# Optimization experiments

Hardware: AMD Instinct MI355X
Metric: run time of the kernel (lower is better)

The kernel has to match this reference:

```python
import math
import jax, jax.numpy as jnp
import numpy as np

HEAD_DIM = 64

def setup_inputs() -> dict:
    key = jax.random.key(0)
    x = jax.random.normal(key, (2, 16, 2048, HEAD_DIM), dtype=jnp.float32)
    return {"x": x}

def reference(x) -> jnp.ndarray:
    D = x.shape[-1]
    rd = math.sqrt(D)            # sqrt(head_dim)
    rrd = math.sqrt(rd)          # head_dim ** 0.25
    r2 = math.sqrt(2.0)
    # outer product over last dim: [..., D, D]
    z = jnp.einsum('...i,...j->...ij', x, x)
    iu, ju = jnp.triu_indices(D, k=1)
    x2_off = z[..., iu, ju]                       # [..., D*(D-1)/2]
    x2_diag = jnp.einsum('...ii->...i', z)        # [..., D]
    ones = jnp.ones_like(x[..., 0:1])
    return jnp.concatenate(
        [ones, x / rrd, x2_diag / (rd * r2), x2_off / rd], axis=-1)
```

## Files before the change

### kernel.cpp

```cpp
#include <hip/hip_runtime.h>


#define D 64
#define ROW 2145
#define OFFD_BASE 129
#define RPB 4

__global__ __launch_bounds__(256) void taylor_fm_kernel(
    const float* __restrict__ x, float* __restrict__ out) {
    __shared__ __align__(16) float buf[RPB * ROW];

    const int wave = threadIdx.x >> 6;
    const int lane = threadIdx.x & 63;
    const int row  = blockIdx.x * RPB + wave;

    const float xl = x[(size_t)row * D + lane];

    const float inv_rrd   = 0.35355339059327373f;
    const float inv_rd_r2 = 0.08838834764831845f;

    float* brow = buf + wave * ROW;
    if (lane == 0) brow[0] = 1.0f;
    brow[1 + lane]  = xl * inv_rrd;
    brow[65 + lane] = xl * xl * inv_rd_r2;

    const float xls = xl * 0.125f;

    float* tri = brow + OFFD_BASE;
#pragma unroll
    for (int i = 0; i < 63; ++i) {
        const int Ci = (i * (127 - i)) >> 1;
        float xi = __uint_as_float(
            __builtin_amdgcn_readlane(__float_as_uint(xls), i));
        if (lane > i) {
            tri[Ci - i - 1 + lane] = xi * xl;
        }
    }

    __syncthreads();

    const float4* b4 = reinterpret_cast<const float4*>(buf);
    float4* o4 = reinterpret_cast<float4*>(out + (size_t)blockIdx.x * (RPB * ROW));
    int q = threadIdx.x;
#pragma unroll
    for (int k = 0; k < 8; ++k, q += 256) {
        o4[q] = b4[q];
    }
    if (q < RPB * ROW / 4) {
        o4[q] = b4[q];
    }
}

extern "C" void kernel_launch(void* const* d_in, const int* in_sizes, int n_in,
                              void* d_out, int out_size, void* d_ws, size_t ws_size,
                              hipStream_t stream) {
    const float* x = (const float*)d_in[0];
    float* out = (float*)d_out;
    int nrows = in_sizes[0] / D;
    taylor_fm_kernel<<<nrows / RPB, 256, 0, stream>>>(x, out);
}
```

Measured before the change: 114.1 us.

## Make blocks persistent over row groups and stage LDS to registers before storing

Each block now loops over 16 groups of 4 rows instead of handling one group. The next row's input is prefetched while the current group is processed. Each group's LDS contents are read into registers, then a barrier frees LDS so the next iteration's compute can overlap with the outstanding global stores. Launch overhead drops 16x, but the grid shrinks to 1024 blocks, which may reduce the parallelism available to saturate write bandwidth on the many CUs.

```diff
diff --git a/kernel.cpp b/kernel.cpp
--- a/kernel.cpp
+++ b/kernel.cpp
@@ -5,6 +5,10 @@
 #define ROW 2145
 #define OFFD_BASE 129
 #define RPB 4
+#define GROUPS 16
+#define NF4 (RPB * ROW / 4)
+
+#define BAR_LGKM() asm volatile("s_waitcnt lgkmcnt(0)\n\ts_barrier" ::: "memory")
 
 __global__ __launch_bounds__(256) void taylor_fm_kernel(
     const float* __restrict__ x, float* __restrict__ out) {
@@ -12,42 +16,53 @@
 
     const int wave = threadIdx.x >> 6;
     const int lane = threadIdx.x & 63;
-    const int row  = blockIdx.x * RPB + wave;
-
-    const float xl = x[(size_t)row * D + lane];
 
     const float inv_rrd   = 0.35355339059327373f;
     const float inv_rd_r2 = 0.08838834764831845f;
 
     float* brow = buf + wave * ROW;
-    if (lane == 0) brow[0] = 1.0f;
-    brow[1 + lane]  = xl * inv_rrd;
-    brow[65 + lane] = xl * xl * inv_rd_r2;
+    float* tri  = brow + OFFD_BASE;
+    const float4* b4 = reinterpret_cast<const float4*>(buf);
 
-    const float xls = xl * 0.125f;
+    int grp = blockIdx.x * GROUPS;
+    float xl = x[((size_t)grp * RPB + wave) * D + lane];
 
-    float* tri = brow + OFFD_BASE;
+    for (int g = 0; g < GROUPS; ++g, ++grp) {
+        if (lane == 0) brow[0] = 1.0f;
+        brow[1 + lane]  = xl * inv_rrd;
+        brow[65 + lane] = xl * xl * inv_rd_r2;
+        const float xls = xl * 0.125f;
 #pragma unroll
-    for (int i = 0; i < 63; ++i) {
-        const int Ci = (i * (127 - i)) >> 1;
-        float xi = __uint_as_float(
-            __builtin_amdgcn_readlane(__float_as_uint(xls), i));
-        if (lane > i) {
-            tri[Ci - i - 1 + lane] = xi * xl;
+        for (int i = 0; i < 63; ++i) {
+            const int Ci = (i * (127 - i)) >> 1;
+            float xi = __uint_as_float(
+                __builtin_amdgcn_readlane(__float_as_uint(xls), i));
+            if (lane > i) {
+                tri[Ci - i - 1 + lane] = xi * xl;
+            }
         }
-    }
+        BAR_LGKM();
 
-    __syncthreads();
+        float xl_next = xl;
+        if (g + 1 < GROUPS) {
+            xl_next = x[((size_t)(grp + 1) * RPB + wave) * D + lane];
+        }
 
-    const float4* b4 = reinterpret_cast<const float4*>(buf);
-    float4* o4 = reinterpret_cast<float4*>(out + (size_t)blockIdx.x * (RPB * ROW));
-    int q = threadIdx.x;
+        float4 r[9];
+        int q = threadIdx.x;
 #pragma unroll
-    for (int k = 0; k < 8; ++k, q += 256) {
-        o4[q] = b4[q];
-    }
-    if (q < RPB * ROW / 4) {
-        o4[q] = b4[q];
+        for (int k = 0; k < 8; ++k, q += 256) r[k] = b4[q];
+        const bool tail = (q < NF4);
+        if (tail) r[8] = b4[q];
+        BAR_LGKM();
+
+        float4* o4 = reinterpret_cast<float4*>(out + (size_t)grp * (RPB * ROW));
+        q = threadIdx.x;
+#pragma unroll
+        for (int k = 0; k < 8; ++k, q += 256) o4[q] = r[k];
+        if (tail) o4[q] = r[8];
+
+        xl = xl_next;
     }
 }
 
@@ -57,5 +72,6 @@
     const float* x = (const float*)d_in[0];
     float* out = (float*)d_out;
     int nrows = in_sizes[0] / D;
-    taylor_fm_kernel<<<nrows / RPB, 256, 0, stream>>>(x, out);
+    int nblocks = nrows / (RPB * GROUPS);
+    taylor_fm_kernel<<<nblocks, 256, 0, stream>>>(x, out);
 }
```

After: 269.9 us. 2.36x slower.

## Switch to persistent single-wave blocks looping over row groups

Applied to the files above, without the earlier changes.

Replaces the one-block-per-4-rows launch of 256 threads with 1024 persistent single-wave blocks. Each block serially builds all 4 rows of a group in LDS and then streams them out with batched float4 loads and stores. The aim is to cut block launch overhead and barrier cost, and to give more stores in flight per wave. The risk is far fewer resident waves per CU, and compute and store phases no longer overlap across waves, which could reduce memory-level parallelism in a kernel that is bound by write bandwidth.

```diff
diff --git a/kernel.cpp b/kernel.cpp
--- a/kernel.cpp
+++ b/kernel.cpp
@@ -5,49 +5,61 @@
 #define ROW 2145
 #define OFFD_BASE 129
 #define RPB 4
+#define CHUNK (RPB * ROW)
+#define NF4 (CHUNK / 4)
+#define NBLOCKS 1024
 
-__global__ __launch_bounds__(256) void taylor_fm_kernel(
-    const float* __restrict__ x, float* __restrict__ out) {
-    __shared__ __align__(16) float buf[RPB * ROW];
-
-    const int wave = threadIdx.x >> 6;
-    const int lane = threadIdx.x & 63;
-    const int row  = blockIdx.x * RPB + wave;
-
-    const float xl = x[(size_t)row * D + lane];
+__global__ __launch_bounds__(64) void taylor_fm_kernel(
+    const float* __restrict__ x, float* __restrict__ out, int ngroups) {
+    __shared__ __align__(16) float buf[CHUNK];
+    const int lane = threadIdx.x;
 
     const float inv_rrd   = 0.35355339059327373f;
     const float inv_rd_r2 = 0.08838834764831845f;
 
-    float* brow = buf + wave * ROW;
-    if (lane == 0) brow[0] = 1.0f;
-    brow[1 + lane]  = xl * inv_rrd;
-    brow[65 + lane] = xl * xl * inv_rd_r2;
+    const float4* b4 = reinterpret_cast<const float4*>(buf);
 
-    const float xls = xl * 0.125f;
+    for (int grp = blockIdx.x; grp < ngroups; grp += NBLOCKS) {
+        const float* xg = x + (size_t)grp * (RPB * D);
+#pragma unroll
+        for (int r = 0; r < RPB; ++r) {
+            const float xl = xg[r * D + lane];
+            float* brow = buf + r * ROW;
+            if (lane == 0) brow[0] = 1.0f;
+            brow[1 + lane]  = xl * inv_rrd;
+            brow[65 + lane] = xl * xl * inv_rd_r2;
+            const float xls = xl * 0.125f;
+            float* tri = brow + OFFD_BASE;
+#pragma unroll
+            for (int i = 0; i < 63; ++i) {
+                const int Ci = (i * (127 - i)) >> 1;
+                float xi = __uint_as_float(
+                    __builtin_amdgcn_readlane(__float_as_uint(xls), i));
+                if (lane > i) {
+                    tri[Ci - i - 1 + lane] = xi * xl;
+                }
+            }
+        }
 
-    float* tri = brow + OFFD_BASE;
+        float4* o4 = reinterpret_cast<float4*>(out + (size_t)grp * CHUNK);
+        int q = lane;
 #pragma unroll
-    for (int i = 0; i < 63; ++i) {
-        const int Ci = (i * (127 - i)) >> 1;
-        float xi = __uint_as_float(
-            __builtin_amdgcn_readlane(__float_as_uint(xls), i));
-        if (lane > i) {
-            tri[Ci - i - 1 + lane] = xi * xl;
+        for (int b = 0; b < 4; ++b) {
+            float4 r0 = b4[q],       r1 = b4[q + 64],  r2 = b4[q + 128],
+                   r3 = b4[q + 192], r4 = b4[q + 256], r5 = b4[q + 320],
+                   r6 = b4[q + 384], r7 = b4[q + 448];
+            o4[q]       = r0; o4[q + 64]  = r1; o4[q + 128] = r2;
+            o4[q + 192] = r3; o4[q + 256] = r4; o4[q + 320] = r5;
+            o4[q + 384] = r6; o4[q + 448] = r7;
+            q += 512;
         }
-    }
-
-    __syncthreads();
-
-    const float4* b4 = reinterpret_cast<const float4*>(buf);
-    float4* o4 = reinterpret_cast<float4*>(out + (size_t)blockIdx.x * (RPB * ROW));
-    int q = threadIdx.x;
-#pragma unroll
-    for (int k = 0; k < 8; ++k, q += 256) {
-        o4[q] = b4[q];
-    }
-    if (q < RPB * ROW / 4) {
-        o4[q] = b4[q];
+        float4 ra = b4[q];
+        o4[q] = ra;
+        q += 64;
+        if (q < NF4) {
+            float4 rb = b4[q];
+            o4[q] = rb;
+        }
     }
 }
 
@@ -57,5 +69,6 @@
     const float* x = (const float*)d_in[0];
     float* out = (float*)d_out;
     int nrows = in_sizes[0] / D;
-    taylor_fm_kernel<<<nrows / RPB, 256, 0, stream>>>(x, out);
+    int ngroups = nrows / RPB;
+    taylor_fm_kernel<<<NBLOCKS, 64, 0, stream>>>(x, out, ngroups);
 }
```

New measurement: 195.1 us. 1.71x slower.
